# Optimization experiments

Measured on AMD Instinct MI355X. Metric: run time of the kernel, lower is better.

The kernel has to match this reference:

```python
import jax, jax.numpy as jnp
import numpy as np

N_SEQ, N_RES, C_M = 512, 256, 256
C_OUTER, C_Z = 32, 128
LN_EPS = 1e-5
NORM_EPS = 1e-3


def setup_inputs() -> dict:
    key = jax.random.key(0)
    ks = jax.random.split(key, 6)
    f32 = jnp.float32
    return {
        "act": jax.random.normal(ks[0], (N_SEQ, N_RES, C_M), f32),
        "mask": jnp.ones((N_SEQ, N_RES), f32),
        # LayerNorm params (create_scale=True, create_offset=True)
        "ln_scale": jnp.ones((C_M,), f32),
        "ln_offset": jnp.zeros((C_M,), f32),
        # left/right projections, 'linear' (VarianceScaling fan_in scale=1)
        "left_w": (jax.random.normal(ks[1], (C_M, C_OUTER), f32) / np.float32(np.sqrt(C_M))),
        "left_b": jnp.zeros((C_OUTER,), f32),
        "right_w": (jax.random.normal(ks[2], (C_M, C_OUTER), f32) / np.float32(np.sqrt(C_M))),
        "right_b": jnp.zeros((C_OUTER,), f32),
        # output_w: VarianceScaling(scale=2.0, fan_in) over (c_outer, c_outer) input dims
        "output_w": (jax.random.normal(ks[3], (C_OUTER, C_OUTER, C_Z), f32)
                     * np.float32(np.sqrt(2.0 / (C_OUTER * C_OUTER)))),
        "output_b": jnp.zeros((C_Z,), f32),
    }


def reference(act, mask, ln_scale, ln_offset, left_w, left_b, right_w, right_b,
              output_w, output_b):
    # LayerNorm over last axis
    mu = jnp.mean(act, axis=-1, keepdims=True)
    var = jnp.var(act, axis=-1, keepdims=True)
    x = (act - mu) * jax.lax.rsqrt(var + LN_EPS) * ln_scale + ln_offset

    m = mask[..., None]  # [N_seq, N_res, 1]
    left = m * (jnp.einsum('abm,mc->abc', x, left_w) + left_b)    # [A,B,Co]
    right = m * (jnp.einsum('abm,me->abe', x, right_w) + right_b)  # [A,D,Co]

    # mean outer product: sum over MSA depth a -> [B, D, Co, Co]
    op = jnp.einsum('abc,ade->bdce', left, right)
    out = jnp.einsum('bdce,cef->bdf', op, output_w) + output_b  # [B, D, Cz]

    # normalization by pairwise mask counts
    norm = jnp.einsum('ab,ad->bd', mask, mask)[..., None]  # [B, D, 1]
    return out / (NORM_EPS + norm)
```

## Files before the change

kernel.cpp:

```cpp
#include <hip/hip_runtime.h>
#include <hip/hip_bf16.h>
#include <stdint.h>

typedef short bf16x8 __attribute__((ext_vector_type(8)));
typedef float f32x4 __attribute__((ext_vector_type(4)));
typedef unsigned short u16x4 __attribute__((ext_vector_type(4)));
typedef unsigned short u16x8 __attribute__((ext_vector_type(8)));

#define GLOAD16(g, l) __builtin_amdgcn_global_load_lds( \
    (const __attribute__((address_space(1))) void*)(g), \
    (__attribute__((address_space(3))) void*)(l), 16, 0, 0)

__device__ __forceinline__ unsigned short f2bf(float f) {
  unsigned u = __float_as_uint(f);
  unsigned r = (u + 0x7fffu + ((u >> 16) & 1u)) >> 16;
  return (unsigned short)r;
}

__global__ __launch_bounds__(256) void prep_k(
    const float* __restrict__ lw, const float* __restrict__ rw,
    const float* __restrict__ ow, unsigned short* __restrict__ Wt,
    unsigned short* __restrict__ wfragG) {
  int idx = blockIdx.x * 256 + threadIdx.x;
  if (idx < 131072) {
    int f = idx >> 10, k2 = idx & 1023;
    int e = k2 >> 5, c = k2 & 31;
    Wt[idx] = f2bf(ow[(size_t)((c << 5) + e) * 128 + f]);
  }
  if (idx < 16384) {
    int frag = idx >> 9, lane = (idx >> 3) & 63, j = idx & 7;
    int wc = frag >> 4, ni = (frag >> 3) & 1, kk = frag & 7;
    int mrow = lane & 15, g = lane >> 4;
    int c = wc * 32 + ni * 16 + mrow;
    int k = kk * 32 + g * 8 + j;
    wfragG[idx] = f2bf(c < 32 ? lw[k * 32 + c] : rw[k * 32 + (c - 32)]);
  }
}

__global__ __launch_bounds__(256) void norm_k(const float* __restrict__ mask,
                                              float* __restrict__ nrm) {
  int b = blockIdx.x, d = threadIdx.x;
  float s = 0.f;
  #pragma unroll 8
  for (int a = 0; a < 512; ++a)
    s += mask[a * 256 + b] * mask[a * 256 + d];
  nrm[(b << 8) + d] = s;
}

__global__ __launch_bounds__(256) void ln_proj(
    const float* __restrict__ act, const float* __restrict__ mask,
    const float* __restrict__ lns, const float* __restrict__ lno,
    const float* __restrict__ lb, const float* __restrict__ rb,
    const unsigned short* __restrict__ wfragG,
    unsigned short* __restrict__ Lt, unsigned short* __restrict__ Rt) {
  __shared__ char smem[32768];
  const int tid = threadIdx.x;
  const int lane = tid & 63;
  const int w = tid >> 6;
  const int b = blockIdx.y;
  const int a0 = blockIdx.x << 6;
  const int r = tid >> 2;
  const int q = tid & 3;

  f32x4 xv[16];
  const float* src = act + ((size_t)(a0 + r) * 256 + b) * 256 + (q << 6);
  #pragma unroll
  for (int i = 0; i < 16; ++i) xv[i] = *(const f32x4*)(src + (i << 2));
  float s = 0.f, sq = 0.f;
  #pragma unroll
  for (int i = 0; i < 16; ++i) {
    f32x4 v = xv[i];
    s += v[0] + v[1] + v[2] + v[3];
    sq += v[0] * v[0] + v[1] * v[1] + v[2] * v[2] + v[3] * v[3];
  }
  s += __shfl_xor(s, 1); sq += __shfl_xor(sq, 1);
  s += __shfl_xor(s, 2); sq += __shfl_xor(sq, 2);
  const float mu = s * (1.f / 256.f);
  const float rs = rsqrtf(sq * (1.f / 256.f) - mu * mu + 1e-5f);

  #pragma unroll
  for (int i = 0; i < 8; ++i) {
    u16x8 pk;
    #pragma unroll
    for (int h = 0; h < 2; ++h) {
      const int b4 = (i << 1) + h;
      const f32x4 sc = *(const f32x4*)(lns + (q << 6) + (b4 << 2));
      const f32x4 of = *(const f32x4*)(lno + (q << 6) + (b4 << 2));
      const f32x4 v = xv[b4];
      #pragma unroll
      for (int jj = 0; jj < 4; ++jj)
        pk[(h << 2) + jj] = f2bf((v[jj] - mu) * rs * sc[jj] + of[jj]);
    }
    const int c = (q << 3) + i;
    *(u16x8*)(smem + (r << 9) + ((c ^ (r & 7)) << 4)) = pk;
  }
  __syncthreads();

  const int wr = w >> 1, wc = w & 1;
  const int mrow = lane & 15, g = lane >> 4;
  f32x4 acc[2][2];
  #pragma unroll
  for (int i = 0; i < 2; ++i)
    #pragma unroll
    for (int jj = 0; jj < 2; ++jj) acc[i][jj] = (f32x4){0.f, 0.f, 0.f, 0.f};
  #pragma unroll
  for (int kk = 0; kk < 8; ++kk) {
    bf16x8 af[2], bfr[2];
    #pragma unroll
    for (int mi = 0; mi < 2; ++mi) {
      const int row = (wr << 5) + (mi << 4) + mrow;
      af[mi] = *(const bf16x8*)(smem + (row << 9) + ((((kk << 2) + g) ^ (row & 7)) << 4));
    }
    #pragma unroll
    for (int ni = 0; ni < 2; ++ni)
      bfr[ni] = *(const bf16x8*)(wfragG + (size_t)((((wc << 1) + ni) << 3) + kk) * 512 + (lane << 3));
    #pragma unroll
    for (int mi = 0; mi < 2; ++mi)
      #pragma unroll
      for (int ni = 0; ni < 2; ++ni)
        acc[mi][ni] = __builtin_amdgcn_mfma_f32_16x16x32_bf16(af[mi], bfr[ni], acc[mi][ni], 0, 0, 0);
  }

  #pragma unroll
  for (int ni = 0; ni < 2; ++ni) {
    const int c31 = (ni << 4) + mrow;
    const float bias = (wc == 0) ? lb[c31] : rb[c31];
    unsigned short* dst = (wc == 0) ? Lt : Rt;
    #pragma unroll
    for (int mi = 0; mi < 2; ++mi) {
      u16x4 pk;
      #pragma unroll
      for (int qq = 0; qq < 4; ++qq) {
        const int ar = (wr << 5) + (mi << 4) + (g << 2) + qq;
        const float mk = mask[(size_t)(a0 + ar) * 256 + b];
        pk[qq] = f2bf((acc[mi][ni][qq] + bias) * mk);
      }
      *(u16x4*)(dst + (size_t)(b * 32 + c31) * 512 + a0 + (wr << 5) + (mi << 4) + (g << 2)) = pk;
    }
  }
}

__global__ __launch_bounds__(512, 2) void gemm_fused(
    const unsigned short* __restrict__ Lt, const unsigned short* __restrict__ Rt,
    const unsigned short* __restrict__ Wt, const float* __restrict__ nrm,
    const float* __restrict__ outb, float* __restrict__ out) {
  __shared__ char smem[131072];
  const int tid = threadIdx.x;
  const int lane = tid & 63;
  const int w = tid >> 6;
  const int wr = w >> 2, wc = w & 3;
  const int mrow = lane & 15, g = lane >> 4;

  const int bid = blockIdx.x;
  const int xcd = bid & 7, jj_ = bid >> 3;
  const int mb = ((jj_ >> 5) << 3) | (jj_ & 7);
  const int nb = (xcd << 2) | ((jj_ >> 3) & 3);
  const int m0i = mb << 8, n0i = nb << 8;

  const int r_l = tid >> 3;
  const int scol = ((tid & 7) ^ (r_l & 7)) << 3;
  const int arow_g = m0i + r_l + ((r_l & 32) ? 96 : 0);

  f32x4 acc[8][4];
  #pragma unroll
  for (int i = 0; i < 8; ++i)
    #pragma unroll
    for (int jj = 0; jj < 4; ++jj) acc[i][jj] = (f32x4){0.f, 0.f, 0.f, 0.f};

  auto STGA = [&](int buf, int p, int kt) {
    GLOAD16(Lt + ((size_t)(arow_g + (p << 5)) << 9) + (kt << 6) + scol,
            smem + buf + (p << 13) + (tid << 4));
  };
  auto STGB = [&](int buf, int q, int kt) {
    GLOAD16(Rt + ((size_t)(n0i + (q << 6) + r_l) << 9) + (kt << 6) + scol,
            smem + buf + 32768 + (q << 13) + (tid << 4));
  };

  #pragma unroll
  for (int p = 0; p < 4; ++p) STGA(0, p, 0);
  #pragma unroll
  for (int qd = 0; qd < 4; ++qd) STGB(0, qd, 0);
  #pragma unroll
  for (int qd = 0; qd < 4; ++qd) STGB(65536, qd, 1);
  STGA(65536, 0, 1); STGA(65536, 1, 1); STGA(65536, 2, 1);
  asm volatile("s_waitcnt vmcnt(7)" ::: "memory");
  __builtin_amdgcn_s_barrier();

  #pragma unroll 1
  for (int t = 0; t < 8; ++t) {
    const int cbuf = (t & 1) << 16;
    const int nbuf = ((t + 1) & 1) << 16;
    bf16x8 bfr[4][2];
    #pragma unroll
    for (int p = 0; p < 4; ++p) {
      bf16x8 af[2][2];
      #pragma unroll
      for (int mi_ = 0; mi_ < 2; ++mi_)
        #pragma unroll
        for (int kk = 0; kk < 2; ++kk) {
          const int loc = (wr << 5) + (mi_ << 4) + mrow;
          af[mi_][kk] = *(const bf16x8*)(smem + cbuf + (p << 13) + (loc << 7) +
                                         ((((kk << 2) + g) ^ (mrow & 7)) << 4));
        }
      if (p == 0) {
        #pragma unroll
        for (int ni = 0; ni < 4; ++ni)
          #pragma unroll
          for (int kk = 0; kk < 2; ++kk) {
            const int loc = (ni << 4) + mrow;
            bfr[ni][kk] = *(const bf16x8*)(smem + cbuf + 32768 + (wc << 13) + (loc << 7) +
                                           ((((kk << 2) + g) ^ (mrow & 7)) << 4));
          }
      }
      if (p == 0) { if (t < 7) STGA(nbuf, 3, t + 1); }
      else if (p == 1) { if (t < 6) { STGB(cbuf, 0, t + 2); STGB(cbuf, 1, t + 2); STGB(cbuf, 2, t + 2); } }
      else if (p == 2) { if (t < 6) { STGB(cbuf, 3, t + 2); STGA(cbuf, 0, t + 2); } }
      else { if (t < 6) { STGA(cbuf, 1, t + 2); STGA(cbuf, 2, t + 2); } }

      __builtin_amdgcn_s_barrier();
      asm volatile("s_waitcnt lgkmcnt(0)" ::: "memory");
      __builtin_amdgcn_sched_barrier(0);
      __builtin_amdgcn_s_setprio(1);
      #pragma unroll
      for (int kk = 0; kk < 2; ++kk)
        #pragma unroll
        for (int mi_ = 0; mi_ < 2; ++mi_)
          #pragma unroll
          for (int ni = 0; ni < 4; ++ni)
            acc[(p << 1) + mi_][ni] = __builtin_amdgcn_mfma_f32_16x16x32_bf16(
                af[mi_][kk], bfr[ni][kk], acc[(p << 1) + mi_][ni], 0, 0, 0);
      __builtin_amdgcn_s_setprio(0);
      if (p == 2) {
        if (t < 6)      asm volatile("s_waitcnt vmcnt(13)" ::: "memory");
        else if (t == 6) asm volatile("s_waitcnt vmcnt(8)" ::: "memory");
        else            asm volatile("s_waitcnt vmcnt(0)" ::: "memory");
      } else if (p == 3) {
        if (t < 6)      asm volatile("s_waitcnt vmcnt(8)" ::: "memory");
        else if (t == 6) asm volatile("s_waitcnt vmcnt(1)" ::: "memory");
      }
      __builtin_amdgcn_s_barrier();
    }
  }

  #pragma unroll
  for (int mi = 0; mi < 8; ++mi) {
    #pragma unroll
    for (int ni = 0; ni < 4; ++ni) {
      const int p = (((wr << 2) + (mi >> 1)) << 3) | ((wc << 1) + (ni >> 1));
      const int ow_ = ((ni & 1) << 10) + (mrow << 6) + ((mi & 1) << 5) + (g << 3);
      u16x4 pk;
      #pragma unroll
      for (int qq = 0; qq < 4; ++qq) pk[qq] = f2bf(acc[mi][ni][qq]);
      *(u16x4*)(smem + (p << 11) + (ow_ ^ ((p & 7) << 4) ^ (((ow_ >> 7) & 7) << 4))) = pk;
    }
  }
  __syncthreads();

  const int f0 = w << 4;
  f32x4 acc2[4];
  #pragma unroll
  for (int i = 0; i < 4; ++i) acc2[i] = (f32x4){0.f, 0.f, 0.f, 0.f};
  const unsigned short* wrow = Wt + (size_t)(f0 + mrow) * 1024;
  #pragma unroll 4
  for (int kk2 = 0; kk2 < 32; ++kk2) {
    const bf16x8 b2 = *(const bf16x8*)(wrow + (kk2 << 5) + (g << 3));
    const int orr = (kk2 << 6) + (g << 4);
    #pragma unroll
    for (int pg = 0; pg < 4; ++pg) {
      const int prow = (pg << 4) + mrow;
      const bf16x8 a2 = *(const bf16x8*)(smem + (prow << 11) +
          (orr ^ ((prow & 7) << 4) ^ (((orr >> 7) & 7) << 4)));
      acc2[pg] = __builtin_amdgcn_mfma_f32_16x16x32_bf16(a2, b2, acc2[pg], 0, 0, 0);
    }
  }

  const float ob_ = outb[f0 + mrow];
  #pragma unroll
  for (int pg = 0; pg < 4; ++pg) {
    #pragma unroll
    for (int qq = 0; qq < 4; ++qq) {
      const int p = (pg << 4) + (g << 2) + qq;
      const int f = f0 + mrow;
      const int bb = (mb << 3) + (p >> 3);
      const int dd = (nb << 3) + (p & 7);
      const float v = acc2[pg][qq] + ob_;
      out[(size_t)((bb << 8) + dd) * 128 + f] = v / (1e-3f + nrm[(bb << 8) + dd]);
    }
  }
}

extern "C" void kernel_launch(void* const* d_in, const int* in_sizes, int n_in,
                              void* d_out, int out_size, void* d_ws, size_t ws_size,
                              hipStream_t stream) {
  const float* act = (const float*)d_in[0];
  const float* mask = (const float*)d_in[1];
  const float* lns = (const float*)d_in[2];
  const float* lno = (const float*)d_in[3];
  const float* lw = (const float*)d_in[4];
  const float* lb = (const float*)d_in[5];
  const float* rw = (const float*)d_in[6];
  const float* rbv = (const float*)d_in[7];
  const float* ow = (const float*)d_in[8];
  const float* ob = (const float*)d_in[9];
  float* out = (float*)d_out;
  char* ws = (char*)d_ws;

  unsigned short* Lt = (unsigned short*)(ws);
  unsigned short* Rt = (unsigned short*)(ws + 8388608);
  unsigned short* Wt = (unsigned short*)(ws + 16777216);
  unsigned short* wfragG = (unsigned short*)(ws + 17039360);
  float* nrm = (float*)(ws + 17072128);

  hipLaunchKernelGGL(prep_k, dim3(512), dim3(256), 0, stream, lw, rw, ow, Wt, wfragG);
  hipLaunchKernelGGL(norm_k, dim3(256), dim3(256), 0, stream, mask, nrm);
  hipLaunchKernelGGL(ln_proj, dim3(8, 256), dim3(256), 0, stream,
                     act, mask, lns, lno, lb, rbv, wfragG, Lt, Rt);
  hipLaunchKernelGGL(gemm_fused, dim3(1024), dim3(512), 0, stream,
                     Lt, Rt, Wt, nrm, ob, out);
}
```

Before: 185.6 us.

## Restructure LN load mapping, stage projection stores via LDS, simplify GEMM pipeline

The LayerNorm stage now has 16 lanes share each row across four row iterations, giving coalesced loads and a lower register footprint, and it sets a launch-bounds occupancy hint. Projection outputs are staged in LDS and written to Lt/Rt as 16-byte row-contiguous stores instead of scattered 8-byte stores. The main GEMM's prefetch schedule is simplified to a plain double buffer with a uniform two-loads-per-phase issue, and the A/B tile assignment is reorganized. The epilogue precomputes reciprocal norms with vector loads and raises the unroll of the second GEMM. These are several independent tweaks, and the pipeline change shortens the prefetch distance, which risks more exposed latency.

```diff
diff --git a/kernel.cpp b/kernel.cpp
--- a/kernel.cpp
+++ b/kernel.cpp
@@ -47,7 +47,7 @@
   nrm[(b << 8) + d] = s;
 }
 
-__global__ __launch_bounds__(256) void ln_proj(
+__global__ __launch_bounds__(256, 4) void ln_proj(
     const float* __restrict__ act, const float* __restrict__ mask,
     const float* __restrict__ lns, const float* __restrict__ lno,
     const float* __restrict__ lb, const float* __restrict__ rb,
@@ -59,40 +59,49 @@
   const int w = tid >> 6;
   const int b = blockIdx.y;
   const int a0 = blockIdx.x << 6;
-  const int r = tid >> 2;
-  const int q = tid & 3;
-
-  f32x4 xv[16];
-  const float* src = act + ((size_t)(a0 + r) * 256 + b) * 256 + (q << 6);
-  #pragma unroll
-  for (int i = 0; i < 16; ++i) xv[i] = *(const f32x4*)(src + (i << 2));
-  float s = 0.f, sq = 0.f;
-  #pragma unroll
-  for (int i = 0; i < 16; ++i) {
-    f32x4 v = xv[i];
-    s += v[0] + v[1] + v[2] + v[3];
-    sq += v[0] * v[0] + v[1] * v[1] + v[2] * v[2] + v[3] * v[3];
-  }
-  s += __shfl_xor(s, 1); sq += __shfl_xor(sq, 1);
-  s += __shfl_xor(s, 2); sq += __shfl_xor(sq, 2);
-  const float mu = s * (1.f / 256.f);
-  const float rs = rsqrtf(sq * (1.f / 256.f) - mu * mu + 1e-5f);
-
-  #pragma unroll
-  for (int i = 0; i < 8; ++i) {
-    u16x8 pk;
-    #pragma unroll
-    for (int h = 0; h < 2; ++h) {
-      const int b4 = (i << 1) + h;
-      const f32x4 sc = *(const f32x4*)(lns + (q << 6) + (b4 << 2));
-      const f32x4 of = *(const f32x4*)(lno + (q << 6) + (b4 << 2));
-      const f32x4 v = xv[b4];
-      #pragma unroll
-      for (int jj = 0; jj < 4; ++jj)
-        pk[(h << 2) + jj] = f2bf((v[jj] - mu) * rs * sc[jj] + of[jj]);
-    }
-    const int c = (q << 3) + i;
-    *(u16x8*)(smem + (r << 9) + ((c ^ (r & 7)) << 4)) = pk;
+  const int l = tid & 15;
+  const int rg = tid >> 4;
+
+  f32x4 sc[4], of[4];
+  #pragma unroll
+  for (int j = 0; j < 4; ++j) {
+    sc[j] = *(const f32x4*)(lns + (l << 4) + (j << 2));
+    of[j] = *(const f32x4*)(lno + (l << 4) + (j << 2));
+  }
+
+  #pragma unroll
+  for (int i = 0; i < 4; ++i) {
+    const int r = rg + (i << 4);
+    const float* src = act + ((size_t)(a0 + r) * 256 + b) * 256 + (l << 4);
+    f32x4 xv[4];
+    #pragma unroll
+    for (int j = 0; j < 4; ++j) xv[j] = *(const f32x4*)(src + (j << 2));
+    float s = 0.f, sq = 0.f;
+    #pragma unroll
+    for (int j = 0; j < 4; ++j) {
+      f32x4 v = xv[j];
+      s += v[0] + v[1] + v[2] + v[3];
+      sq += v[0] * v[0] + v[1] * v[1] + v[2] * v[2] + v[3] * v[3];
+    }
+    s += __shfl_xor(s, 1); sq += __shfl_xor(sq, 1);
+    s += __shfl_xor(s, 2); sq += __shfl_xor(sq, 2);
+    s += __shfl_xor(s, 4); sq += __shfl_xor(sq, 4);
+    s += __shfl_xor(s, 8); sq += __shfl_xor(sq, 8);
+    const float mu = s * (1.f / 256.f);
+    const float rs = rsqrtf(sq * (1.f / 256.f) - mu * mu + 1e-5f);
+    #pragma unroll
+    for (int hh = 0; hh < 2; ++hh) {
+      u16x8 pk;
+      #pragma unroll
+      for (int j2 = 0; j2 < 2; ++j2) {
+        const int j = (hh << 1) + j2;
+        #pragma unroll
+        for (int e = 0; e < 4; ++e)
+          pk[(j2 << 2) + e] = f2bf((xv[j][e] - mu) * rs * sc[j][e] + of[j][e]);
+      }
+      const int c = (l << 1) + hh;
+      *(u16x8*)(smem + (r << 9) + ((c ^ (r & 7)) << 4)) = pk;
+    }
   }
   __syncthreads();
 
@@ -120,23 +129,33 @@
       for (int ni = 0; ni < 2; ++ni)
         acc[mi][ni] = __builtin_amdgcn_mfma_f32_16x16x32_bf16(af[mi], bfr[ni], acc[mi][ni], 0, 0, 0);
   }
+  __syncthreads();
 
   #pragma unroll
   for (int ni = 0; ni < 2; ++ni) {
-    const int c31 = (ni << 4) + mrow;
-    const float bias = (wc == 0) ? lb[c31] : rb[c31];
-    unsigned short* dst = (wc == 0) ? Lt : Rt;
+    const int c = (wc << 5) + (ni << 4) + mrow;
+    const float bias = (wc == 0) ? lb[(ni << 4) + mrow] : rb[(ni << 4) + mrow];
     #pragma unroll
     for (int mi = 0; mi < 2; ++mi) {
+      const int aB = (wr << 5) + (mi << 4) + (g << 2);
       u16x4 pk;
       #pragma unroll
       for (int qq = 0; qq < 4; ++qq) {
-        const int ar = (wr << 5) + (mi << 4) + (g << 2) + qq;
-        const float mk = mask[(size_t)(a0 + ar) * 256 + b];
+        const float mk = mask[(size_t)(a0 + aB + qq) * 256 + b];
         pk[qq] = f2bf((acc[mi][ni][qq] + bias) * mk);
       }
-      *(u16x4*)(dst + (size_t)(b * 32 + c31) * 512 + a0 + (wr << 5) + (mi << 4) + (g << 2)) = pk;
-    }
+      *(u16x4*)(smem + (c << 7) + ((((aB >> 3) & 7) ^ (c & 7)) << 4) + ((aB & 7) << 1)) = pk;
+    }
+  }
+  __syncthreads();
+
+  #pragma unroll
+  for (int s = 0; s < 2; ++s) {
+    const int c = (w << 4) + (s << 3) + (lane >> 3);
+    const int gr = lane & 7;
+    const u16x8 v = *(const u16x8*)(smem + (c << 7) + ((gr ^ (c & 7)) << 4));
+    unsigned short* dst = (c < 32) ? Lt : Rt;
+    *(u16x8*)(dst + (size_t)(b * 32 + (c & 31)) * 512 + a0 + (gr << 3)) = v;
   }
 }
 
@@ -157,9 +176,7 @@
   const int nb = (xcd << 2) | ((jj_ >> 3) & 3);
   const int m0i = mb << 8, n0i = nb << 8;
 
-  const int r_l = tid >> 3;
-  const int scol = ((tid & 7) ^ (r_l & 7)) << 3;
-  const int arow_g = m0i + r_l + ((r_l & 32) ? 96 : 0);
+  const int scol = (((tid & 7) ^ ((tid >> 3) & 7)) << 3);
 
   f32x4 acc[8][4];
   #pragma unroll
@@ -167,76 +184,63 @@
     #pragma unroll
     for (int jj = 0; jj < 4; ++jj) acc[i][jj] = (f32x4){0.f, 0.f, 0.f, 0.f};
 
-  auto STGA = [&](int buf, int p, int kt) {
-    GLOAD16(Lt + ((size_t)(arow_g + (p << 5)) << 9) + (kt << 6) + scol,
-            smem + buf + (p << 13) + (tid << 4));
+  auto STG = [&](const unsigned short* gsrc, int baserow, int dstoff, int kt) {
+    GLOAD16(gsrc + ((size_t)(baserow + (tid >> 3)) << 9) + (kt << 6) + scol,
+            smem + dstoff + (tid << 4));
   };
-  auto STGB = [&](int buf, int q, int kt) {
-    GLOAD16(Rt + ((size_t)(n0i + (q << 6) + r_l) << 9) + (kt << 6) + scol,
-            smem + buf + 32768 + (q << 13) + (tid << 4));
-  };
-
-  #pragma unroll
-  for (int p = 0; p < 4; ++p) STGA(0, p, 0);
-  #pragma unroll
-  for (int qd = 0; qd < 4; ++qd) STGB(0, qd, 0);
-  #pragma unroll
-  for (int qd = 0; qd < 4; ++qd) STGB(65536, qd, 1);
-  STGA(65536, 0, 1); STGA(65536, 1, 1); STGA(65536, 2, 1);
-  asm volatile("s_waitcnt vmcnt(7)" ::: "memory");
+
+  STG(Rt, n0i, 32768, 0);        STG(Rt, n0i + 64, 40960, 0);
+  STG(Rt, n0i + 128, 49152, 0);  STG(Rt, n0i + 192, 57344, 0);
+  STG(Lt, m0i, 0, 0);            STG(Lt, m0i + 128, 16384, 0);
+  STG(Lt, m0i + 64, 8192, 0);    STG(Lt, m0i + 192, 24576, 0);
+  asm volatile("s_waitcnt vmcnt(2)" ::: "memory");
   __builtin_amdgcn_s_barrier();
 
   #pragma unroll 1
   for (int t = 0; t < 8; ++t) {
     const int cbuf = (t & 1) << 16;
     const int nbuf = ((t + 1) & 1) << 16;
+    const int k1 = t + 1;
+    const bool pfe = (t < 7);
     bf16x8 bfr[4][2];
     #pragma unroll
     for (int p = 0; p < 4; ++p) {
-      bf16x8 af[2][2];
-      #pragma unroll
-      for (int mi_ = 0; mi_ < 2; ++mi_)
-        #pragma unroll
-        for (int kk = 0; kk < 2; ++kk) {
-          const int loc = (wr << 5) + (mi_ << 4) + mrow;
-          af[mi_][kk] = *(const bf16x8*)(smem + cbuf + (p << 13) + (loc << 7) +
-                                         ((((kk << 2) + g) ^ (mrow & 7)) << 4));
-        }
-      if (p == 0) {
+      const int h = p >> 1, kk = p & 1;
+      bf16x8 af[4];
+      #pragma unroll
+      for (int mi_ = 0; mi_ < 4; ++mi_) {
+        af[mi_] = *(const bf16x8*)(smem + cbuf + (((wr << 1) + h) << 13) +
+                                   (((mi_ << 4) + mrow) << 7) +
+                                   ((((kk << 2) + g) ^ (mrow & 7)) << 4));
+      }
+      if (p < 2) {
         #pragma unroll
         for (int ni = 0; ni < 4; ++ni)
-          #pragma unroll
-          for (int kk = 0; kk < 2; ++kk) {
-            const int loc = (ni << 4) + mrow;
-            bfr[ni][kk] = *(const bf16x8*)(smem + cbuf + 32768 + (wc << 13) + (loc << 7) +
-                                           ((((kk << 2) + g) ^ (mrow & 7)) << 4));
-          }
-      }
-      if (p == 0) { if (t < 7) STGA(nbuf, 3, t + 1); }
-      else if (p == 1) { if (t < 6) { STGB(cbuf, 0, t + 2); STGB(cbuf, 1, t + 2); STGB(cbuf, 2, t + 2); } }
-      else if (p == 2) { if (t < 6) { STGB(cbuf, 3, t + 2); STGA(cbuf, 0, t + 2); } }
-      else { if (t < 6) { STGA(cbuf, 1, t + 2); STGA(cbuf, 2, t + 2); } }
-
-      __builtin_amdgcn_s_barrier();
+          bfr[ni][p] = *(const bf16x8*)(smem + cbuf + 32768 + (wc << 13) +
+                                        (((ni << 4) + mrow) << 7) +
+                                        ((((p << 2) + g) ^ (mrow & 7)) << 4));
+      }
+      if (pfe) {
+        if (p == 0)      { STG(Rt, n0i, nbuf + 32768, k1);       STG(Rt, n0i + 64, nbuf + 40960, k1); }
+        else if (p == 1) { STG(Rt, n0i + 128, nbuf + 49152, k1); STG(Rt, n0i + 192, nbuf + 57344, k1); }
+        else if (p == 2) { STG(Lt, m0i, nbuf, k1);               STG(Lt, m0i + 128, nbuf + 16384, k1); }
+        else             { STG(Lt, m0i + 64, nbuf + 8192, k1);   STG(Lt, m0i + 192, nbuf + 24576, k1); }
+      }
       asm volatile("s_waitcnt lgkmcnt(0)" ::: "memory");
       __builtin_amdgcn_sched_barrier(0);
       __builtin_amdgcn_s_setprio(1);
       #pragma unroll
-      for (int kk = 0; kk < 2; ++kk)
+      for (int mi_ = 0; mi_ < 4; ++mi_)
         #pragma unroll
-        for (int mi_ = 0; mi_ < 2; ++mi_)
-          #pragma unroll
-          for (int ni = 0; ni < 4; ++ni)
-            acc[(p << 1) + mi_][ni] = __builtin_amdgcn_mfma_f32_16x16x32_bf16(
-                af[mi_][kk], bfr[ni][kk], acc[(p << 1) + mi_][ni], 0, 0, 0);
+        for (int ni = 0; ni < 4; ++ni)
+          acc[(h << 2) + mi_][ni] = __builtin_amdgcn_mfma_f32_16x16x32_bf16(
+              af[mi_], bfr[ni][kk], acc[(h << 2) + mi_][ni], 0, 0, 0);
       __builtin_amdgcn_s_setprio(0);
-      if (p == 2) {
-        if (t < 6)      asm volatile("s_waitcnt vmcnt(13)" ::: "memory");
-        else if (t == 6) asm volatile("s_waitcnt vmcnt(8)" ::: "memory");
-        else            asm volatile("s_waitcnt vmcnt(0)" ::: "memory");
-      } else if (p == 3) {
-        if (t < 6)      asm volatile("s_waitcnt vmcnt(8)" ::: "memory");
-        else if (t == 6) asm volatile("s_waitcnt vmcnt(1)" ::: "memory");
+      if (p == 1) {
+        if (t < 7) asm volatile("s_waitcnt vmcnt(4)" ::: "memory");
+        else       asm volatile("s_waitcnt vmcnt(0)" ::: "memory");
+      } else if (p == 3 && pfe) {
+        asm volatile("s_waitcnt vmcnt(2)" ::: "memory");
       }
       __builtin_amdgcn_s_barrier();
     }
@@ -256,12 +260,21 @@
   }
   __syncthreads();
 
+  f32x4 invn[4];
+  #pragma unroll
+  for (int pg = 0; pg < 4; ++pg) {
+    const int bb = (mb << 3) + (pg << 1) + (g >> 1);
+    const f32x4 nv = *(const f32x4*)(nrm + (bb << 8) + (nb << 3) + ((g & 1) << 2));
+    #pragma unroll
+    for (int qq = 0; qq < 4; ++qq) invn[pg][qq] = __builtin_amdgcn_rcpf(1e-3f + nv[qq]);
+  }
+
   const int f0 = w << 4;
   f32x4 acc2[4];
   #pragma unroll
   for (int i = 0; i < 4; ++i) acc2[i] = (f32x4){0.f, 0.f, 0.f, 0.f};
   const unsigned short* wrow = Wt + (size_t)(f0 + mrow) * 1024;
-  #pragma unroll 4
+  #pragma unroll 8
   for (int kk2 = 0; kk2 < 32; ++kk2) {
     const bf16x8 b2 = *(const bf16x8*)(wrow + (kk2 << 5) + (g << 3));
     const int orr = (kk2 << 6) + (g << 4);
@@ -280,11 +293,9 @@
     #pragma unroll
     for (int qq = 0; qq < 4; ++qq) {
       const int p = (pg << 4) + (g << 2) + qq;
-      const int f = f0 + mrow;
       const int bb = (mb << 3) + (p >> 3);
       const int dd = (nb << 3) + (p & 7);
-      const float v = acc2[pg][qq] + ob_;
-      out[(size_t)((bb << 8) + dd) * 128 + f] = v / (1e-3f + nrm[(bb << 8) + dd]);
+      out[(size_t)((bb << 8) + dd) * 128 + f0 + mrow] = (acc2[pg][qq] + ob_) * invn[pg][qq];
     }
   }
 }
```

New measurement: 158.6 us. 1.17x faster.
